# Kernel optimization log

Hardware: AMD Instinct MI355X
Metric: run time of the kernel (lower is better)

The kernel has to match this reference:

```python
import jax, jax.numpy as jnp
import numpy as np


def _apply_rope(x, rope):
    # x: (B, T, D); rope: (T, D//2, 2) broadcast over batch
    B, T, D = x.shape
    x_ = x.reshape(B, T, D // 2, 2)
    cos, sin = rope[..., 0], rope[..., 1]
    xr, xi = x_[..., 0], x_[..., 1]
    rotr = xr * cos - xi * sin
    roti = xr * sin + xi * cos
    return jnp.stack([rotr, roti], axis=-1).reshape(B, T, D)


def setup_inputs() -> dict:
    key = jax.random.key(0)
    k1, k2, k3, k4 = jax.random.split(key, 4)
    B, T, D, H = 2, 2048, 1024, 16
    x = jax.random.normal(k1, (B, T, D), dtype=jnp.float32)
    rope = jax.random.normal(k2, (T, D // 2, 2), dtype=jnp.float32)
    w_qkv = jax.random.normal(k3, (3 * D, D), dtype=jnp.float32) * (1.0 / np.sqrt(D))
    w_proj = jax.random.normal(k4, (D, D), dtype=jnp.float32) * (1.0 / np.sqrt(D))
    return {"x": x, "rope": rope, "w_qkv": w_qkv, "w_proj": w_proj}


def reference(x, rope, w_qkv, w_proj):
    B, T, D = x.shape
    H = 16
    dk = D // H
    qkv = jnp.einsum("btd,ed->bte", x, w_qkv)  # (B, T, 3D)
    q, k, v = jnp.split(qkv, 3, axis=-1)
    q = _apply_rope(q, rope)
    k = _apply_rope(k, rope)
    # split heads: (B, H, T, dk)
    q = q.reshape(B, T, H, dk).transpose(0, 2, 1, 3)
    k = k.reshape(B, T, H, dk).transpose(0, 2, 1, 3)
    v = v.reshape(B, T, H, dk).transpose(0, 2, 1, 3)
    att = jnp.einsum("bhqd,bhkd->bhqk", q, k) / jnp.sqrt(jnp.float32(dk)).astype(x.dtype)
    att = jax.nn.softmax(att, axis=-1)
    out = jnp.einsum("bhqk,bhkd->bhqd", att, v)
    out = out.transpose(0, 2, 1, 3).reshape(B, T, D)
    return jnp.einsum("btd,ed->bte", out, w_proj)
```

## Files before the change

kernel.cpp:

```cpp
#include <hip/hip_runtime.h>

typedef _Float16 f16;
typedef _Float16 f16x2 __attribute__((ext_vector_type(2)));
typedef _Float16 f16x4 __attribute__((ext_vector_type(4)));
typedef _Float16 f16x8 __attribute__((ext_vector_type(8)));
typedef float    f32x2 __attribute__((ext_vector_type(2)));
typedef float    f32x4 __attribute__((ext_vector_type(4)));
typedef short    s16x4 __attribute__((ext_vector_type(4)));

#define GLDS16(gptr, lptr)                                                     \
  __builtin_amdgcn_global_load_lds(                                            \
      (const __attribute__((address_space(1))) void*)(gptr),                   \
      (__attribute__((address_space(3))) void*)(lptr), 16, 0, 0)

#define S_BARRIER() __builtin_amdgcn_s_barrier()
#define FENCE() asm volatile("" ::: "memory")
#define WAIT_VM8() asm volatile("s_waitcnt vmcnt(8)" ::: "memory")
#define WAIT_VM0() asm volatile("s_waitcnt vmcnt(0)" ::: "memory")
#define WAIT_LGKM0() asm volatile("s_waitcnt lgkmcnt(0)" ::: "memory")

__device__ inline short f32_to_bf16_rne(float f) {
  unsigned u = __builtin_bit_cast(unsigned, f);
  return (short)((u + 0x7FFFu + ((u >> 16) & 1u)) >> 16);
}

__global__ __launch_bounds__(256) void k_cast3(const float* __restrict__ a,
                                               const float* __restrict__ b,
                                               const float* __restrict__ c,
                                               f16* __restrict__ oa,
                                               f16* __restrict__ ob,
                                               f16* __restrict__ oc) {
  int i = blockIdx.x * 256 + threadIdx.x;
  const float* src;
  f16* dst;
  int off;
  if (i < 1048576) { src = a; dst = oa; off = i; }
  else if (i < 1835008) { src = b; dst = ob; off = i - 1048576; }
  else { src = c; dst = oc; off = i - 1835008; }
  f32x4 v = ((const f32x4*)src)[off];
  f16x4 h;
  h[0] = (f16)v[0]; h[1] = (f16)v[1]; h[2] = (f16)v[2]; h[3] = (f16)v[3];
  ((f16x4*)dst)[off] = h;
}

__global__ __launch_bounds__(256, 4) void k_gemm_qkv(
    const f16* __restrict__ A, const f16* __restrict__ B,
    const float* __restrict__ rope, f16* __restrict__ qh,
    f16* __restrict__ kh, short* __restrict__ vt) {
  const int K = 1024;
  __shared__ f16 sA[128 * 64];
  __shared__ f16 sB[128 * 64];
  const int tid = threadIdx.x;
  const int wave = tid >> 6, lane = tid & 63;
  const int lr = lane & 15, lq = lane >> 4;
  const int lr7 = lr & 7;
  const int wm = (wave >> 1) * 64, wn = (wave & 1) * 64;
  const size_t m0 = (size_t)blockIdx.x * 128, n0 = (size_t)blockIdx.y * 128;

  f32x4 acc[4][4] = {};

  const int sw8 = ((tid & 7) ^ ((tid >> 3) & 7)) * 8;
  const f16* ga = A + (m0 + (tid >> 3)) * (size_t)K + sw8;
  const f16* gb = B + (n0 + (tid >> 3)) * (size_t)K + sw8;

  for (int k0 = 0; k0 < K; k0 += 64) {
    __syncthreads();
#pragma unroll
    for (int r = 0; r < 4; ++r) {
      GLDS16(ga + (size_t)(r * 32) * K + k0, (char*)sA + r * 4096 + wave * 1024);
      GLDS16(gb + (size_t)(r * 32) * K + k0, (char*)sB + r * 4096 + wave * 1024);
    }
    __syncthreads();

#pragma unroll
    for (int kk = 0; kk < 2; ++kk) {
      f16x8 af[4], bf[4];
#pragma unroll
      for (int i = 0; i < 4; ++i)
        af[i] = *(const f16x8*)&sA[(wm + i * 16 + lr) * 64 +
                                   (((kk * 4 + lq) ^ lr7) * 8)];
#pragma unroll
      for (int j = 0; j < 4; ++j)
        bf[j] = *(const f16x8*)&sB[(wn + j * 16 + lr) * 64 +
                                   (((kk * 4 + lq) ^ lr7) * 8)];
#pragma unroll
      for (int i = 0; i < 4; ++i)
#pragma unroll
        for (int j = 0; j < 4; ++j)
          acc[i][j] = __builtin_amdgcn_mfma_f32_16x16x32_f16(af[i], bf[j],
                                                             acc[i][j], 0, 0, 0);
    }
  }

  const int region = (int)(n0 >> 10);
  if (region == 2) {
#pragma unroll
    for (int i = 0; i < 4; ++i)
#pragma unroll
      for (int j = 0; j < 4; ++j) {
        int e = (int)(n0 + wn + j * 16 + lr) - 2048;
        int h = e >> 6, c = e & 63;
        int m = (int)(m0 + wm + i * 16 + lq * 4);
        int b = m >> 11, t0 = m & 2047;
        s16x4 o;
#pragma unroll
        for (int r = 0; r < 4; ++r) o[r] = f32_to_bf16_rne(acc[i][j][r]);
        *(s16x4*)&vt[(((size_t)(b * 16 + h)) * 64 + c) * 2048 + t0] = o;
      }
  } else {
    const float scl = region == 0 ? 0.1803368801111204f : 1.0f;
    f16* dst = region == 0 ? qh : kh;
    const int odd = lr & 1;
#pragma unroll
    for (int i = 0; i < 4; ++i)
#pragma unroll
      for (int j = 0; j < 4; ++j) {
        int e = ((int)(n0 + wn + j * 16 + lr)) & 1023;
        int h = e >> 6, c = e & 63, p = e >> 1;
        int mb = (int)(m0 + wm + i * 16 + lq * 4);
        int b = mb >> 11;
#pragma unroll
        for (int r = 0; r < 4; ++r) {
          int t = (mb + r) & 2047;
          float v = acc[i][j][r];
          float partner = __shfl_xor(v, 1);
          f32x2 cs = *(const f32x2*)&rope[((size_t)t * 512 + p) * 2];
          float out = odd ? (partner * cs[1] + v * cs[0])
                          : (v * cs[0] - partner * cs[1]);
          dst[(((size_t)(b * 16 + h)) * 2048 + t) * 64 + c] = (f16)(out * scl);
        }
      }
  }
}

__global__ __launch_bounds__(256, 4) void k_gemm_bt(const f16* __restrict__ A,
                                                    const f16* __restrict__ B,
                                                    float* __restrict__ C,
                                                    int M, int N, int K) {
  __shared__ f16 sA[128 * 64];
  __shared__ f16 sB[128 * 64];
  const int tid = threadIdx.x;
  const int wave = tid >> 6, lane = tid & 63;
  const int lr = lane & 15, lq = lane >> 4;
  const int lr7 = lr & 7;
  const int wm = (wave >> 1) * 64, wn = (wave & 1) * 64;
  const size_t m0 = (size_t)blockIdx.x * 128, n0 = (size_t)blockIdx.y * 128;

  f32x4 acc[4][4] = {};

  const int sw8 = ((tid & 7) ^ ((tid >> 3) & 7)) * 8;
  const f16* ga = A + (m0 + (tid >> 3)) * (size_t)K + sw8;
  const f16* gb = B + (n0 + (tid >> 3)) * (size_t)K + sw8;

  for (int k0 = 0; k0 < K; k0 += 64) {
    __syncthreads();
#pragma unroll
    for (int r = 0; r < 4; ++r) {
      GLDS16(ga + (size_t)(r * 32) * K + k0, (char*)sA + r * 4096 + wave * 1024);
      GLDS16(gb + (size_t)(r * 32) * K + k0, (char*)sB + r * 4096 + wave * 1024);
    }
    __syncthreads();

#pragma unroll
    for (int kk = 0; kk < 2; ++kk) {
      f16x8 af[4], bf[4];
#pragma unroll
      for (int i = 0; i < 4; ++i)
        af[i] = *(const f16x8*)&sA[(wm + i * 16 + lr) * 64 +
                                   (((kk * 4 + lq) ^ lr7) * 8)];
#pragma unroll
      for (int j = 0; j < 4; ++j)
        bf[j] = *(const f16x8*)&sB[(wn + j * 16 + lr) * 64 +
                                   (((kk * 4 + lq) ^ lr7) * 8)];
#pragma unroll
      for (int i = 0; i < 4; ++i)
#pragma unroll
        for (int j = 0; j < 4; ++j)
          acc[i][j] = __builtin_amdgcn_mfma_f32_16x16x32_f16(af[i], bf[j],
                                                             acc[i][j], 0, 0, 0);
    }
  }

#pragma unroll
  for (int i = 0; i < 4; ++i)
#pragma unroll
    for (int j = 0; j < 4; ++j)
#pragma unroll
      for (int r = 0; r < 4; ++r)
        C[(m0 + wm + i * 16 + lq * 4 + r) * (size_t)N + n0 + wn + j * 16 + lr] =
            acc[i][j][r];
}

__global__ __launch_bounds__(256, 2) void k_attn(const f16* __restrict__ Qp,
                                                 const f16* __restrict__ Kp,
                                                 const short* __restrict__ Vt,
                                                 f16* __restrict__ Op) {
  __shared__ f16 sQ[128 * 64];
  __shared__ f16 sKV[2 * 16384];
  const int tid = threadIdx.x, wave = tid >> 6, lane = tid & 63;
  const int lr = lane & 15, lq = lane >> 4;
  const int lr7 = lr & 7;
  const int bh = blockIdx.x, qt = blockIdx.y;
  const size_t base = (size_t)bh * 2048 * 64;

  const int sw8 = ((tid & 7) ^ ((tid >> 3) & 7)) * 8;
  const int sw16 = ((tid & 15) ^ ((tid >> 4) & 15)) * 8;

  auto stage_kv = [&](int jcc, int d) {
    const f16* gk = Kp + base + (size_t)jcc * 128 * 64;
    const short* gv = Vt + base + (size_t)jcc * 128;
    char* bK = (char*)sKV + d * 32768;
    char* bV = bK + 16384;
#pragma unroll
    for (int r = 0; r < 4; ++r) {
      GLDS16(gk + (size_t)(r * 32 + (tid >> 3)) * 64 + sw8,
             bK + r * 4096 + wave * 1024);
      GLDS16(gv + (size_t)(r * 16 + (tid >> 4)) * 2048 + sw16,
             bV + r * 4096 + wave * 1024);
    }
  };

  const f16* gq = Qp + base + (size_t)qt * 128 * 64;
#pragma unroll
  for (int r = 0; r < 4; ++r)
    GLDS16(gq + (size_t)(r * 32 + (tid >> 3)) * 64 + sw8,
           (char*)sQ + r * 4096 + wave * 1024);
  stage_kv(0, 0);
  WAIT_VM8();
  S_BARRIER();
  FENCE();
  f16x8 qa0 = *(const f16x8*)&sQ[(wave * 32 + lr) * 64 + ((lq ^ lr7) * 8)];
  f16x8 qa1 = *(const f16x8*)&sQ[(wave * 32 + lr) * 64 + (((4 + lq) ^ lr7) * 8)];
  f16x8 qb0 = *(const f16x8*)&sQ[(wave * 32 + 16 + lr) * 64 + ((lq ^ lr7) * 8)];
  f16x8 qb1 =
      *(const f16x8*)&sQ[(wave * 32 + 16 + lr) * 64 + (((4 + lq) ^ lr7) * 8)];

  f32x4 ota[4] = {}, otb[4] = {};
  float la = 0.f, lb = 0.f;

#pragma unroll 1
  for (int jc = 0; jc < 16; ++jc) {
    const int cur = jc & 1;
    if (jc < 15) {
      stage_kv(jc + 1, cur ^ 1);
      WAIT_VM8();
    } else {
      WAIT_VM0();
    }
    S_BARRIER();
    FENCE();

    const f16* bK = (const f16*)((char*)sKV + cur * 32768);
    const short* bV = (const short*)((char*)sKV + cur * 32768 + 16384);

    s16x4 pfa[8], pfb[8];
#pragma unroll
    for (int nt = 0; nt < 8; ++nt) {
      f16x8 kf0 = *(const f16x8*)&bK[(nt * 16 + lr) * 64 + ((lq ^ lr7) * 8)];
      f16x8 kf1 =
          *(const f16x8*)&bK[(nt * 16 + lr) * 64 + (((4 + lq) ^ lr7) * 8)];
      f32x4 z = {0.f, 0.f, 0.f, 0.f};
      f32x4 sa = __builtin_amdgcn_mfma_f32_16x16x32_f16(kf0, qa0, z, 0, 0, 0);
      sa = __builtin_amdgcn_mfma_f32_16x16x32_f16(kf1, qa1, sa, 0, 0, 0);
      f32x4 sb = __builtin_amdgcn_mfma_f32_16x16x32_f16(kf0, qb0, z, 0, 0, 0);
      sb = __builtin_amdgcn_mfma_f32_16x16x32_f16(kf1, qb1, sb, 0, 0, 0);
#pragma unroll
      for (int r = 0; r < 4; ++r) {
        float pa = __builtin_amdgcn_exp2f(sa[r]);
        float pb = __builtin_amdgcn_exp2f(sb[r]);
        la += pa; lb += pb;
        pfa[nt][r] = (short)(__builtin_bit_cast(unsigned, pa) >> 16);
        pfb[nt][r] = (short)(__builtin_bit_cast(unsigned, pb) >> 16);
      }
    }

#pragma unroll
    for (int d = 0; d < 4; ++d)
#pragma unroll
      for (int ks = 0; ks < 8; ++ks) {
        int vslot = (ks * 2 + (lq >> 1)) ^ lr;
        s16x4 vf = *(const s16x4*)&bV[(d * 16 + lr) * 128 + vslot * 8 +
                                      (lq & 1) * 4];
        ota[d] = __builtin_amdgcn_mfma_f32_16x16x16bf16_1k(vf, pfa[ks], ota[d],
                                                           0, 0, 0);
        otb[d] = __builtin_amdgcn_mfma_f32_16x16x16bf16_1k(vf, pfb[ks], otb[d],
                                                           0, 0, 0);
      }

    WAIT_LGKM0();
    S_BARRIER();
    FENCE();
  }

  la += __shfl_xor(la, 16); la += __shfl_xor(la, 32);
  lb += __shfl_xor(lb, 16); lb += __shfl_xor(lb, 32);
  float rla = 1.f / la, rlb = 1.f / lb;
  int b = bh >> 4, h = bh & 15;
  int ta = qt * 128 + wave * 32 + lr;
  f16* gouta = Op + ((size_t)(b * 2048 + ta)) * 1024 + h * 64;
  f16* goutb = gouta + (size_t)16 * 1024;
#pragma unroll
  for (int d = 0; d < 4; ++d) {
    f16x4 oa, ob;
#pragma unroll
    for (int r = 0; r < 4; ++r) {
      oa[r] = (f16)(ota[d][r] * rla);
      ob[r] = (f16)(otb[d][r] * rlb);
    }
    *(f16x4*)&gouta[d * 16 + lq * 4] = oa;
    *(f16x4*)&goutb[d * 16 + lq * 4] = ob;
  }
}

extern "C" void kernel_launch(void* const* d_in, const int* in_sizes, int n_in,
                              void* d_out, int out_size, void* d_ws,
                              size_t ws_size, hipStream_t stream) {
  const float* x     = (const float*)d_in[0];
  const float* rope  = (const float*)d_in[1];
  const float* wqkv  = (const float*)d_in[2];
  const float* wproj = (const float*)d_in[3];
  float* out = (float*)d_out;

  char* w = (char*)d_ws;
  const size_t MB = 1024 * 1024;
  f16* xh   = (f16*)(w + 0);
  f16* wqh  = (f16*)(w + 8 * MB);
  f16* wph  = (f16*)(w + 14 * MB);
  f16* qh   = (f16*)(w + 16 * MB);
  f16* kh   = (f16*)(w + 24 * MB);
  short* vth = (short*)(w + 32 * MB);
  f16* aoh  = (f16*)(w + 40 * MB);

  k_cast3<<<8192, 256, 0, stream>>>(x, wqkv, wproj, xh, wqh, wph);

  k_gemm_qkv<<<dim3(32, 24), 256, 0, stream>>>(xh, wqh, rope, qh, kh, vth);

  k_attn<<<dim3(32, 16), 256, 0, stream>>>(qh, kh, vth, aoh);

  k_gemm_bt<<<dim3(32, 8), 256, 0, stream>>>(aoh, wph, out, 4096, 1024, 1024);
}
```

Baseline: 181.8 us.

## Single-buffer K/V tiles in attention to fit three blocks per CU

The attention kernel drops the double-buffered K/V staging in shared memory and uses one K buffer and one V buffer. It loads the next tile synchronously between two __syncthreads barriers at the end of each iteration. The smaller LDS footprint, together with launch bounds raised from 2 to 3, is meant to let more blocks share a CU, so latency is hidden by other blocks rather than by in-block prefetch. The trade-off is that each block's global loads no longer overlap its own MFMA work, and the tighter register budget may cause spills.

```diff
diff --git a/kernel.cpp b/kernel.cpp
--- a/kernel.cpp
+++ b/kernel.cpp
@@ -12,12 +12,6 @@
   __builtin_amdgcn_global_load_lds(                                            \
       (const __attribute__((address_space(1))) void*)(gptr),                   \
       (__attribute__((address_space(3))) void*)(lptr), 16, 0, 0)
-
-#define S_BARRIER() __builtin_amdgcn_s_barrier()
-#define FENCE() asm volatile("" ::: "memory")
-#define WAIT_VM8() asm volatile("s_waitcnt vmcnt(8)" ::: "memory")
-#define WAIT_VM0() asm volatile("s_waitcnt vmcnt(0)" ::: "memory")
-#define WAIT_LGKM0() asm volatile("s_waitcnt lgkmcnt(0)" ::: "memory")
 
 __device__ inline short f32_to_bf16_rne(float f) {
   unsigned u = __builtin_bit_cast(unsigned, f);
@@ -191,12 +185,13 @@
             acc[i][j][r];
 }
 
-__global__ __launch_bounds__(256, 2) void k_attn(const f16* __restrict__ Qp,
+__global__ __launch_bounds__(256, 3) void k_attn(const f16* __restrict__ Qp,
                                                  const f16* __restrict__ Kp,
                                                  const short* __restrict__ Vt,
                                                  f16* __restrict__ Op) {
   __shared__ f16 sQ[128 * 64];
-  __shared__ f16 sKV[2 * 16384];
+  __shared__ f16 sK[128 * 64];
+  __shared__ short sV[64 * 128];
   const int tid = threadIdx.x, wave = tid >> 6, lane = tid & 63;
   const int lr = lane & 15, lq = lane >> 4;
   const int lr7 = lr & 7;
@@ -206,29 +201,23 @@
   const int sw8 = ((tid & 7) ^ ((tid >> 3) & 7)) * 8;
   const int sw16 = ((tid & 15) ^ ((tid >> 4) & 15)) * 8;
 
-  auto stage_kv = [&](int jcc, int d) {
-    const f16* gk = Kp + base + (size_t)jcc * 128 * 64;
-    const short* gv = Vt + base + (size_t)jcc * 128;
-    char* bK = (char*)sKV + d * 32768;
-    char* bV = bK + 16384;
-#pragma unroll
-    for (int r = 0; r < 4; ++r) {
-      GLDS16(gk + (size_t)(r * 32 + (tid >> 3)) * 64 + sw8,
-             bK + r * 4096 + wave * 1024);
-      GLDS16(gv + (size_t)(r * 16 + (tid >> 4)) * 2048 + sw16,
-             bV + r * 4096 + wave * 1024);
-    }
-  };
-
   const f16* gq = Qp + base + (size_t)qt * 128 * 64;
 #pragma unroll
   for (int r = 0; r < 4; ++r)
     GLDS16(gq + (size_t)(r * 32 + (tid >> 3)) * 64 + sw8,
            (char*)sQ + r * 4096 + wave * 1024);
-  stage_kv(0, 0);
-  WAIT_VM8();
-  S_BARRIER();
-  FENCE();
+  {
+    const f16* gk = Kp + base;
+    const short* gv = Vt + base;
+#pragma unroll
+    for (int r = 0; r < 4; ++r) {
+      GLDS16(gk + (size_t)(r * 32 + (tid >> 3)) * 64 + sw8,
+             (char*)sK + r * 4096 + wave * 1024);
+      GLDS16(gv + (size_t)(r * 16 + (tid >> 4)) * 2048 + sw16,
+             (char*)sV + r * 4096 + wave * 1024);
+    }
+  }
+  __syncthreads();
   f16x8 qa0 = *(const f16x8*)&sQ[(wave * 32 + lr) * 64 + ((lq ^ lr7) * 8)];
   f16x8 qa1 = *(const f16x8*)&sQ[(wave * 32 + lr) * 64 + (((4 + lq) ^ lr7) * 8)];
   f16x8 qb0 = *(const f16x8*)&sQ[(wave * 32 + 16 + lr) * 64 + ((lq ^ lr7) * 8)];
@@ -240,25 +229,12 @@
 
 #pragma unroll 1
   for (int jc = 0; jc < 16; ++jc) {
-    const int cur = jc & 1;
-    if (jc < 15) {
-      stage_kv(jc + 1, cur ^ 1);
-      WAIT_VM8();
-    } else {
-      WAIT_VM0();
-    }
-    S_BARRIER();
-    FENCE();
-
-    const f16* bK = (const f16*)((char*)sKV + cur * 32768);
-    const short* bV = (const short*)((char*)sKV + cur * 32768 + 16384);
-
     s16x4 pfa[8], pfb[8];
 #pragma unroll
     for (int nt = 0; nt < 8; ++nt) {
-      f16x8 kf0 = *(const f16x8*)&bK[(nt * 16 + lr) * 64 + ((lq ^ lr7) * 8)];
+      f16x8 kf0 = *(const f16x8*)&sK[(nt * 16 + lr) * 64 + ((lq ^ lr7) * 8)];
       f16x8 kf1 =
-          *(const f16x8*)&bK[(nt * 16 + lr) * 64 + (((4 + lq) ^ lr7) * 8)];
+          *(const f16x8*)&sK[(nt * 16 + lr) * 64 + (((4 + lq) ^ lr7) * 8)];
       f32x4 z = {0.f, 0.f, 0.f, 0.f};
       f32x4 sa = __builtin_amdgcn_mfma_f32_16x16x32_f16(kf0, qa0, z, 0, 0, 0);
       sa = __builtin_amdgcn_mfma_f32_16x16x32_f16(kf1, qa1, sa, 0, 0, 0);
@@ -279,7 +255,7 @@
 #pragma unroll
       for (int ks = 0; ks < 8; ++ks) {
         int vslot = (ks * 2 + (lq >> 1)) ^ lr;
-        s16x4 vf = *(const s16x4*)&bV[(d * 16 + lr) * 128 + vslot * 8 +
+        s16x4 vf = *(const s16x4*)&sV[(d * 16 + lr) * 128 + vslot * 8 +
                                       (lq & 1) * 4];
         ota[d] = __builtin_amdgcn_mfma_f32_16x16x16bf16_1k(vf, pfa[ks], ota[d],
                                                            0, 0, 0);
@@ -287,9 +263,19 @@
                                                            0, 0, 0);
       }
 
-    WAIT_LGKM0();
-    S_BARRIER();
-    FENCE();
+    if (jc < 15) {
+      __syncthreads();
+      const f16* gk = Kp + base + (size_t)(jc + 1) * 128 * 64;
+      const short* gv = Vt + base + (size_t)(jc + 1) * 128;
+#pragma unroll
+      for (int r = 0; r < 4; ++r) {
+        GLDS16(gk + (size_t)(r * 32 + (tid >> 3)) * 64 + sw8,
+               (char*)sK + r * 4096 + wave * 1024);
+        GLDS16(gv + (size_t)(r * 16 + (tid >> 4)) * 2048 + sw16,
+               (char*)sV + r * 4096 + wave * 1024);
+      }
+      __syncthreads();
+    }
   }
 
   la += __shfl_xor(la, 16); la += __shfl_xor(la, 32);
```

Result: slower. 200.8 us (+10.4%).
